# Performance work log

Hardware: AMD Instinct MI355X
Metric: run time of the kernel (lower is better)

## Reference

```python
import jax, jax.numpy as jnp
import numpy as np

INPUT_SIZE = 64
HIDDEN = 512
NUM_CLASSES = 10


def setup_inputs() -> dict:
    key = jax.random.key(0)
    ks = jax.random.split(key, 9)
    B, T = 1024, 256
    bound_lstm = 1.0 / np.sqrt(HIDDEN)
    bound_lin = 1.0 / np.sqrt(HIDDEN)
    x = jax.random.normal(ks[0], (B, T * INPUT_SIZE), dtype=jnp.float32)
    h0 = jax.random.normal(ks[1], (B, HIDDEN), dtype=jnp.float32)
    c0 = jax.random.normal(ks[2], (B, HIDDEN), dtype=jnp.float32)
    W_ih = jax.random.uniform(ks[3], (4 * HIDDEN, INPUT_SIZE), jnp.float32, -bound_lstm, bound_lstm)
    W_hh = jax.random.uniform(ks[4], (4 * HIDDEN, HIDDEN), jnp.float32, -bound_lstm, bound_lstm)
    b_ih = jax.random.uniform(ks[5], (4 * HIDDEN,), jnp.float32, -bound_lstm, bound_lstm)
    b_hh = jax.random.uniform(ks[6], (4 * HIDDEN,), jnp.float32, -bound_lstm, bound_lstm)
    W_lin = jax.random.uniform(ks[7], (NUM_CLASSES, HIDDEN), jnp.float32, -bound_lin, bound_lin)
    b_lin = jax.random.uniform(ks[8], (NUM_CLASSES,), jnp.float32, -bound_lin, bound_lin)
    return {"x": x, "h0": h0, "c0": c0, "W_ih": W_ih, "W_hh": W_hh,
            "b_ih": b_ih, "b_hh": b_hh, "W_lin": W_lin, "b_lin": b_lin}


def _lstm_forward(x, h0, c0, W_ih, W_hh, b_ih, b_hh, W_lin, b_lin):
    B = x.shape[0]
    T = x.shape[1] // INPUT_SIZE
    # [B, T*in] -> [T, B, in]; torch.split along dim 1 gives contiguous chunks
    xs = x.reshape(B, T, INPUT_SIZE).transpose(1, 0, 2)
    # precompute input projections for all steps: [T, B, 4H]
    gates_x = jnp.einsum('tbi,gi->tbg', xs, W_ih) + b_ih + b_hh

    def step(carry, gx):
        h, c = carry
        gates = gx + h @ W_hh.T  # [B, 4H], torch gate order i,f,g,o
        i, f, g, o = jnp.split(gates, 4, axis=-1)
        i = jax.nn.sigmoid(i)
        f = jax.nn.sigmoid(f)
        g = jnp.tanh(g)
        o = jax.nn.sigmoid(o)
        c_new = f * c + i * g
        h_new = o * jnp.tanh(c_new)
        return (h_new, c_new), None

    (hT, cT), _ = jax.lax.scan(step, (h0, c0), gates_x)
    preds = hT @ W_lin.T + b_lin  # [B, 10]
    return preds


def reference(x, h0, c0, W_ih, W_hh, b_ih, b_hh, W_lin, b_lin):
    return _lstm_forward(x, h0, c0, W_ih, W_hh, b_ih, b_hh, W_lin, b_lin)
```

## Files before the change

### kernel.cpp

```cpp
#include <hip/hip_runtime.h>
#include <hip/hip_bf16.h>


#define TST   256
#define BATCH 1024
#define HID   512
#define INSZ  64
#define NCLS  10
#define LDSTR 584

typedef _Float16 f16x8  __attribute__((ext_vector_type(8)));
typedef float    f32x16 __attribute__((ext_vector_type(16)));
typedef unsigned long long u64;

__device__ __forceinline__ float fast_rcp(float x) {
    return __builtin_amdgcn_rcpf(x);
}

__device__ __forceinline__ float tanh_f(float x) {
    return 2.0f * fast_rcp(1.0f + __expf(-2.0f * x)) - 1.0f;
}

__device__ __forceinline__ f16x8 cvt8(float4 a, float4 b) {
    f16x8 o;
    o[0] = (_Float16)a.x; o[1] = (_Float16)a.y; o[2] = (_Float16)a.z; o[3] = (_Float16)a.w;
    o[4] = (_Float16)b.x; o[5] = (_Float16)b.y; o[6] = (_Float16)b.z; o[7] = (_Float16)b.w;
    return o;
}

__device__ __forceinline__ u64 cvt4_u64(float4 a) {
    _Float16 h[4] = {(_Float16)a.x, (_Float16)a.y, (_Float16)a.z, (_Float16)a.w};
    u64 r;
    __builtin_memcpy(&r, h, 8);
    return r;
}

template <int CTRL>
__device__ __forceinline__ float dpp_f(float v) {
    return __builtin_bit_cast(float,
        __builtin_amdgcn_mov_dpp(__builtin_bit_cast(int, v), CTRL, 0xF, 0xF, true));
}
template <int CTRL>
__device__ __forceinline__ unsigned dpp_u(unsigned v) {
    return (unsigned)__builtin_amdgcn_mov_dpp((int)v, CTRL, 0xF, 0xF, true);
}

__global__ __launch_bounds__(256, 1) void lstm_persist(
    const float* __restrict__ x,   const float* __restrict__ h0,
    const float* __restrict__ c0,  const float* __restrict__ Wih,
    const float* __restrict__ Whh, const float* __restrict__ bih,
    const float* __restrict__ bhh, _Float16* __restrict__ hb,
    unsigned* __restrict__ bar)
{
    __shared__ __align__(16) _Float16 As[32][LDSTR];

    const int tid   = threadIdx.x;
    const int lane  = tid & 63;
    const int w     = tid >> 6;
    const int l31   = lane & 31;
    const int khalf = (lane >> 5) * 8;
    const int g  = (int)(blockIdx.x >> 3);
    const int jb = (int)(blockIdx.x & 7);
    const int m0 = g * 32;
    const int j0 = jb * 64;
    unsigned* flg = bar + g * 64;

    const int gate = l31 & 3;
    int jcol[2], nrow[2];
    #pragma unroll
    for (int nt = 0; nt < 2; ++nt) {
        int np = w * 64 + nt * 32 + l31;
        jcol[nt] = j0 + (np >> 2);
        nrow[nt] = gate * HID + jcol[nt];
    }

    f16x8 bfr[2][36];
    #pragma unroll
    for (int nt = 0; nt < 2; ++nt)
        #pragma unroll
        for (int kt = 0; kt < 36; ++kt) {
            const int k0 = kt * 16 + khalf;
            const float* p = (kt < 32) ? (Whh + (size_t)nrow[nt] * HID + k0)
                                       : (Wih + (size_t)nrow[nt] * INSZ + (k0 - HID));
            float4 f0 = ((const float4*)p)[0];
            float4 f1 = ((const float4*)p)[1];
            bfr[nt][kt] = cvt8(f0, f1);
        }
    float bsv[2];
    bsv[0] = bih[nrow[0]] + bhh[nrow[0]];
    bsv[1] = bih[nrow[1]] + bhh[nrow[1]];
    const float s   = (gate == 2) ? 2.0f : 1.0f;
    const int rowhi = (lane >> 5) * 4;

    float cr[2][16];
    #pragma unroll
    for (int nt = 0; nt < 2; ++nt)
        #pragma unroll
        for (int r = 0; r < 16; ++r) {
            int row = (r & 3) + 8 * (r >> 2) + rowhi;
            cr[nt][r] = c0[(size_t)(m0 + row) * HID + jcol[nt]];
        }

    const int rr = tid >> 3;
    const int q  = tid & 7;

    for (int t = 0; t < TST; ++t) {
        const _Float16* rb = hb + (size_t)((t + 2) % 3) * (BATCH * HID);
        _Float16*       wb = hb + (size_t)(t % 3) * (BATCH * HID);

        float4 x0, x1;
        {
            const float* xp = x + (size_t)(m0 + rr) * (TST * INSZ) + t * INSZ + q * 8;
            x0 = ((const float4*)xp)[0];
            x1 = ((const float4*)xp)[1];
        }
        if (t == 0) {
            u64 hv[16];
            #pragma unroll
            for (int u = 0; u < 16; ++u) {
                float4 f = *(const float4*)(h0 + (size_t)(m0 + rr) * HID + q * 4 + u * 32);
                hv[u] = cvt4_u64(f);
            }
            #pragma unroll
            for (int u = 0; u < 16; ++u)
                *(u64*)&As[rr][q * 4 + u * 32] = hv[u];
        } else {
            const unsigned tgt = (unsigned)t;
            int spins = 0;
            while (true) {
                unsigned v = tgt;
                if (lane < 32)
                    v = __hip_atomic_load(flg + lane,
                                          __ATOMIC_RELAXED, __HIP_MEMORY_SCOPE_AGENT);
                if (__all((int)(v >= tgt))) break;
                if (++spins > (1 << 16)) break;
                __builtin_amdgcn_s_sleep(1);
            }
            __atomic_signal_fence(__ATOMIC_SEQ_CST);
            const u64* rbq = (const u64*)(rb + (size_t)(m0 + rr) * HID);
            u64 hv[16];
            #pragma unroll
            for (int u = 0; u < 16; ++u)
                hv[u] = __hip_atomic_load(&rbq[q + u * 8],
                                          __ATOMIC_RELAXED, __HIP_MEMORY_SCOPE_AGENT);
            #pragma unroll
            for (int u = 0; u < 16; ++u)
                *(u64*)&As[rr][q * 4 + u * 32] = hv[u];
        }
        *(f16x8*)&As[rr][512 + q * 8] = cvt8(x0, x1);
        __syncthreads();

        f32x16 acc[2];
        #pragma unroll
        for (int i = 0; i < 16; ++i) { acc[0][i] = 0.0f; acc[1][i] = 0.0f; }
        #pragma unroll
        for (int kt = 0; kt < 36; ++kt) {
            f16x8 af = *(const f16x8*)&As[l31][kt * 16 + khalf];
            acc[0] = __builtin_amdgcn_mfma_f32_32x32x16_f16(af, bfr[0][kt], acc[0], 0, 0, 0);
            acc[1] = __builtin_amdgcn_mfma_f32_32x32x16_f16(af, bfr[1][kt], acc[1], 0, 0, 0);
        }

        #pragma unroll
        for (int nt = 0; nt < 2; ++nt) {
            #pragma unroll
            for (int r = 0; r < 16; ++r) {
                float v = acc[nt][r] + bsv[nt];
                float e = __expf(-s * v);
                float act = s * fast_rcp(1.0f + e) - (s - 1.0f);
                float fu = dpp_f<0xB1>(act);
                float gu = dpp_f<0x4E>(act);
                float ou = dpp_f<0x1B>(act);
                float cn = fu * cr[nt][r] + act * gu;
                cr[nt][r] = cn;
                float hn = ou * tanh_f(cn);
                unsigned hu = (unsigned)__builtin_bit_cast(unsigned short, (_Float16)hn);
                unsigned pk = hu | (dpp_u<0x104>(hu) << 16);
                u64 v4 = (u64)pk | ((u64)dpp_u<0x108>(pk) << 32);
                if ((l31 & 15) == 0) {
                    int row = (r & 3) + 8 * (r >> 2) + rowhi;
                    __hip_atomic_store((u64*)&wb[(size_t)(m0 + row) * HID + jcol[nt]],
                                       v4, __ATOMIC_RELAXED, __HIP_MEMORY_SCOPE_AGENT);
                }
            }
        }

        asm volatile("s_waitcnt vmcnt(0)" ::: "memory");
        if (lane == 0)
            __hip_atomic_store(flg + (jb * 4 + w), (unsigned)(t + 1),
                               __ATOMIC_RELAXED, __HIP_MEMORY_SCOPE_AGENT);
    }
}

__global__ __launch_bounds__(256) void final_kernel(
    const _Float16* __restrict__ h, const float* __restrict__ Wl,
    const float* __restrict__ bl, float* __restrict__ out)
{
    int i = blockIdx.x * 256 + threadIdx.x;
    if (i >= BATCH * NCLS) return;
    int b = i / NCLS, c = i - b * NCLS;
    const f16x8* hp = (const f16x8*)(h + (size_t)b * HID);
    const float4* wp = (const float4*)(Wl + (size_t)c * HID);
    float sacc = bl[c];
    #pragma unroll 4
    for (int k8 = 0; k8 < HID / 8; ++k8) {
        f16x8 hv = hp[k8];
        float4 w0 = wp[2 * k8], w1 = wp[2 * k8 + 1];
        sacc += (float)hv[0] * w0.x + (float)hv[1] * w0.y +
                (float)hv[2] * w0.z + (float)hv[3] * w0.w +
                (float)hv[4] * w1.x + (float)hv[5] * w1.y +
                (float)hv[6] * w1.z + (float)hv[7] * w1.w;
    }
    out[i] = sacc;
}

extern "C" void kernel_launch(void* const* d_in, const int* in_sizes, int n_in,
                              void* d_out, int out_size, void* d_ws, size_t ws_size,
                              hipStream_t stream)
{
    const float* x    = (const float*)d_in[0];
    const float* h0   = (const float*)d_in[1];
    const float* c0   = (const float*)d_in[2];
    const float* Wih  = (const float*)d_in[3];
    const float* Whh  = (const float*)d_in[4];
    const float* bih  = (const float*)d_in[5];
    const float* bhh  = (const float*)d_in[6];
    const float* Wlin = (const float*)d_in[7];
    const float* blin = (const float*)d_in[8];
    float* out = (float*)d_out;

    unsigned* bar = (unsigned*)d_ws;
    _Float16* hb  = (_Float16*)((char*)d_ws + 8192);

    hipMemsetAsync(d_ws, 0, 8192, stream);

    lstm_persist<<<256, 256, 0, stream>>>(x, h0, c0, Wih, Whh, bih, bhh, hb, bar);

    final_kernel<<<(BATCH * NCLS + 255) / 256, 256, 0, stream>>>(hb, Wlin, blin, out);
}
```

Before: 1.715 ms.

## Split persistent LSTM across 512 blocks with one MFMA tile per wave

Each block now owns 32 hidden columns instead of 64, so every wave computes a single 32x32 gate tile. This halves the serial MFMA chain and the register-held weight fragments per wave. The grid doubles to 512 blocks with two blocks per CU, and the per-group flag barrier now polls 64 flags instead of 32. In exchange, each block still stages the full h row tile from global memory every step, which doubles global h reads, and the spin-wait timeout is shortened.

```diff
diff --git a/kernel.cpp b/kernel.cpp
--- a/kernel.cpp
+++ b/kernel.cpp
@@ -45,7 +45,7 @@
     return (unsigned)__builtin_amdgcn_mov_dpp((int)v, CTRL, 0xF, 0xF, true);
 }
 
-__global__ __launch_bounds__(256, 1) void lstm_persist(
+__global__ __launch_bounds__(256, 2) void lstm_persist(
     const float* __restrict__ x,   const float* __restrict__ h0,
     const float* __restrict__ c0,  const float* __restrict__ Wih,
     const float* __restrict__ Whh, const float* __restrict__ bih,
@@ -59,47 +59,36 @@
     const int w     = tid >> 6;
     const int l31   = lane & 31;
     const int khalf = (lane >> 5) * 8;
-    const int g  = (int)(blockIdx.x >> 3);
-    const int jb = (int)(blockIdx.x & 7);
+    const int g  = (int)(blockIdx.x >> 4);
+    const int jb = (int)(blockIdx.x & 15);
     const int m0 = g * 32;
-    const int j0 = jb * 64;
+    const int j0 = jb * 32;
     unsigned* flg = bar + g * 64;
 
     const int gate = l31 & 3;
-    int jcol[2], nrow[2];
+    const int jcol = j0 + w * 8 + (l31 >> 2);
+    const int nrow = gate * HID + jcol;
+
+    f16x8 bfr[36];
     #pragma unroll
-    for (int nt = 0; nt < 2; ++nt) {
-        int np = w * 64 + nt * 32 + l31;
-        jcol[nt] = j0 + (np >> 2);
-        nrow[nt] = gate * HID + jcol[nt];
-    }
-
-    f16x8 bfr[2][36];
-    #pragma unroll
-    for (int nt = 0; nt < 2; ++nt)
-        #pragma unroll
-        for (int kt = 0; kt < 36; ++kt) {
-            const int k0 = kt * 16 + khalf;
-            const float* p = (kt < 32) ? (Whh + (size_t)nrow[nt] * HID + k0)
-                                       : (Wih + (size_t)nrow[nt] * INSZ + (k0 - HID));
-            float4 f0 = ((const float4*)p)[0];
-            float4 f1 = ((const float4*)p)[1];
-            bfr[nt][kt] = cvt8(f0, f1);
-        }
-    float bsv[2];
-    bsv[0] = bih[nrow[0]] + bhh[nrow[0]];
-    bsv[1] = bih[nrow[1]] + bhh[nrow[1]];
+    for (int kt = 0; kt < 36; ++kt) {
+        const int k0 = kt * 16 + khalf;
+        const float* p = (kt < 32) ? (Whh + (size_t)nrow * HID + k0)
+                                   : (Wih + (size_t)nrow * INSZ + (k0 - HID));
+        float4 f0 = ((const float4*)p)[0];
+        float4 f1 = ((const float4*)p)[1];
+        bfr[kt] = cvt8(f0, f1);
+    }
+    const float bsv = bih[nrow] + bhh[nrow];
     const float s   = (gate == 2) ? 2.0f : 1.0f;
     const int rowhi = (lane >> 5) * 4;
 
-    float cr[2][16];
+    float cr[16];
     #pragma unroll
-    for (int nt = 0; nt < 2; ++nt)
-        #pragma unroll
-        for (int r = 0; r < 16; ++r) {
-            int row = (r & 3) + 8 * (r >> 2) + rowhi;
-            cr[nt][r] = c0[(size_t)(m0 + row) * HID + jcol[nt]];
-        }
+    for (int r = 0; r < 16; ++r) {
+        int row = (r & 3) + 8 * (r >> 2) + rowhi;
+        cr[r] = c0[(size_t)(m0 + row) * HID + jcol];
+    }
 
     const int rr = tid >> 3;
     const int q  = tid & 7;
@@ -128,12 +117,10 @@
             const unsigned tgt = (unsigned)t;
             int spins = 0;
             while (true) {
-                unsigned v = tgt;
-                if (lane < 32)
-                    v = __hip_atomic_load(flg + lane,
-                                          __ATOMIC_RELAXED, __HIP_MEMORY_SCOPE_AGENT);
+                unsigned v = __hip_atomic_load(flg + lane,
+                                               __ATOMIC_RELAXED, __HIP_MEMORY_SCOPE_AGENT);
                 if (__all((int)(v >= tgt))) break;
-                if (++spins > (1 << 16)) break;
+                if (++spins > (1 << 14)) break;
                 __builtin_amdgcn_s_sleep(1);
             }
             __atomic_signal_fence(__ATOMIC_SEQ_CST);
@@ -150,37 +137,33 @@
         *(f16x8*)&As[rr][512 + q * 8] = cvt8(x0, x1);
         __syncthreads();
 
-        f32x16 acc[2];
+        f32x16 acc;
         #pragma unroll
-        for (int i = 0; i < 16; ++i) { acc[0][i] = 0.0f; acc[1][i] = 0.0f; }
+        for (int i = 0; i < 16; ++i) acc[i] = 0.0f;
         #pragma unroll
         for (int kt = 0; kt < 36; ++kt) {
             f16x8 af = *(const f16x8*)&As[l31][kt * 16 + khalf];
-            acc[0] = __builtin_amdgcn_mfma_f32_32x32x16_f16(af, bfr[0][kt], acc[0], 0, 0, 0);
-            acc[1] = __builtin_amdgcn_mfma_f32_32x32x16_f16(af, bfr[1][kt], acc[1], 0, 0, 0);
+            acc = __builtin_amdgcn_mfma_f32_32x32x16_f16(af, bfr[kt], acc, 0, 0, 0);
         }
 
         #pragma unroll
-        for (int nt = 0; nt < 2; ++nt) {
-            #pragma unroll
-            for (int r = 0; r < 16; ++r) {
-                float v = acc[nt][r] + bsv[nt];
-                float e = __expf(-s * v);
-                float act = s * fast_rcp(1.0f + e) - (s - 1.0f);
-                float fu = dpp_f<0xB1>(act);
-                float gu = dpp_f<0x4E>(act);
-                float ou = dpp_f<0x1B>(act);
-                float cn = fu * cr[nt][r] + act * gu;
-                cr[nt][r] = cn;
-                float hn = ou * tanh_f(cn);
-                unsigned hu = (unsigned)__builtin_bit_cast(unsigned short, (_Float16)hn);
-                unsigned pk = hu | (dpp_u<0x104>(hu) << 16);
-                u64 v4 = (u64)pk | ((u64)dpp_u<0x108>(pk) << 32);
-                if ((l31 & 15) == 0) {
-                    int row = (r & 3) + 8 * (r >> 2) + rowhi;
-                    __hip_atomic_store((u64*)&wb[(size_t)(m0 + row) * HID + jcol[nt]],
-                                       v4, __ATOMIC_RELAXED, __HIP_MEMORY_SCOPE_AGENT);
-                }
+        for (int r = 0; r < 16; ++r) {
+            float v = acc[r] + bsv;
+            float e = __expf(-s * v);
+            float act = s * fast_rcp(1.0f + e) - (s - 1.0f);
+            float fu = dpp_f<0xB1>(act);
+            float gu = dpp_f<0x4E>(act);
+            float ou = dpp_f<0x1B>(act);
+            float cn = fu * cr[r] + act * gu;
+            cr[r] = cn;
+            float hn = ou * tanh_f(cn);
+            unsigned hu = (unsigned)__builtin_bit_cast(unsigned short, (_Float16)hn);
+            unsigned pk = hu | (dpp_u<0x104>(hu) << 16);
+            u64 v4 = (u64)pk | ((u64)dpp_u<0x108>(pk) << 32);
+            if ((l31 & 15) == 0) {
+                int row = (r & 3) + 8 * (r >> 2) + rowhi;
+                __hip_atomic_store((u64*)&wb[(size_t)(m0 + row) * HID + jcol],
+                                   v4, __ATOMIC_RELAXED, __HIP_MEMORY_SCOPE_AGENT);
             }
         }
 
@@ -233,7 +216,7 @@
 
     hipMemsetAsync(d_ws, 0, 8192, stream);
 
-    lstm_persist<<<256, 256, 0, stream>>>(x, h0, c0, Wih, Whh, bih, bhh, hb, bar);
+    lstm_persist<<<512, 256, 0, stream>>>(x, h0, c0, Wih, Whh, bih, bhh, hb, bar);
 
     final_kernel<<<(BATCH * NCLS + 255) / 256, 256, 0, stream>>>(hb, Wlin, blin, out);
 }
```

After: 2.081 ms. +21.4%, slower.
